# Performance work log

Hardware: AMD Instinct MI355X
Metric: run time of the kernel (lower is better)

Reference implementation:

```python
import jax, jax.numpy as jnp
import numpy as np

B, T, D, V = 32, 384, 768, 32000
PAD = 1
THRESH = 0.95

def setup_inputs() -> dict:
    key = jax.random.key(0)
    ks = jax.random.split(key, 8)
    s = 1.0 / np.sqrt(D)
    sentence = jax.random.randint(ks[0], (B, T), 0, V)
    emb = jax.random.normal(ks[1], (V, D), jnp.float32) * 0.02
    emb = emb.at[PAD].set(0.0)  # padding_idx row is zero
    w_ih = jax.random.uniform(ks[2], (3 * D, D), jnp.float32, -s, s)
    w_hh = jax.random.uniform(ks[3], (3 * D, D), jnp.float32, -s, s)
    b_ih = jax.random.uniform(ks[4], (3 * D,), jnp.float32, -s, s)
    b_hh = jax.random.uniform(ks[5], (3 * D,), jnp.float32, -s, s)
    w_act = jax.random.uniform(ks[6], (D,), jnp.float32, -s, s)
    b_act = jnp.zeros((1,), jnp.float32)
    return dict(sentence=sentence, emb=emb, w_ih=w_ih, w_hh=w_hh,
                b_ih=b_ih, b_hh=b_hh, w_act=w_act, b_act=b_act)


def _gru(x, w_ih, w_hh, b_ih, b_hh):
    # x: [B,T,D] -> states [B,T,D]; PyTorch GRU cell math.
    xp = jnp.einsum('btd,ed->bte', x, w_ih) + b_ih  # [B,T,3D]

    def step(h, xt):
        hp = h @ w_hh.T + b_hh
        xr, xz, xn = jnp.split(xt, 3, axis=-1)
        hr, hz, hn = jnp.split(hp, 3, axis=-1)
        r = jax.nn.sigmoid(xr + hr)
        z = jax.nn.sigmoid(xz + hz)
        n = jnp.tanh(xn + r * hn)
        h_new = (1.0 - z) * n + z * h
        return h_new, h_new

    h0 = jnp.zeros((x.shape[0], w_hh.shape[1]), x.dtype)
    _, hs = jax.lax.scan(step, h0, jnp.swapaxes(xp, 0, 1))
    return jnp.swapaxes(hs, 0, 1)


def _forward(sentence, emb, w_ih, w_hh, b_ih, b_hh, w_act, b_act):
    x = emb[sentence]                                   # [B,T,D]
    states = _gru(x, w_ih, w_hh, b_ih, b_hh)            # [B,T,D]
    probs = jax.nn.sigmoid(states @ w_act + b_act)      # [B,T]

    # ACT-style halting: accumulate probs, emit a segment when sum > threshold.
    def halt_step(hsum, p):
        acc = hsum + p
        halted = acc > THRESH
        return jnp.where(halted, 0.0, acc), halted

    _, halted_t = jax.lax.scan(halt_step, jnp.zeros((B,), probs.dtype), probs.T)
    halted = halted_t.T                                 # [B,T] bool, True at last step of each segment
    h_i = halted.astype(jnp.int32)
    seg_id = jnp.cumsum(h_i, axis=1) - h_i              # exclusive cumsum: segment index per step

    segsum = jax.vmap(lambda v, s: jax.ops.segment_sum(v, s, num_segments=T))
    sum_p = segsum(probs, seg_id)                       # [B,T] per-segment prob sum
    sum_p_at = jnp.take_along_axis(sum_p, seg_id, axis=1)
    # last step of a segment gets weight p_last - stopgrad(sum_seg - 1)
    weights = jnp.where(halted, probs - jax.lax.stop_gradient(sum_p_at - 1.0), probs)
    seg_embs = segsum(states * weights[..., None], seg_id)  # [B,T,D]

    n_segs = h_i.sum(axis=1)                            # [B] completed segments
    valid = jnp.arange(T)[None, :] < n_segs[:, None]    # [B,T]
    embs = jnp.where(valid[..., None], seg_embs, 0.0)   # zero-pad incomplete slots
    embs = embs.reshape(B * T, D)                       # concat padded per-batch lists
    return embs, probs[..., None]


def reference(sentence, emb, w_ih, w_hh, b_ih, b_hh, w_act, b_act):
    return _forward(sentence, emb, w_ih, w_hh, b_ih, b_hh, w_act, b_act)
```

## Files before the change

### kernel.cpp

```cpp
#include <hip/hip_runtime.h>
#include <math.h>

#define BATCH 32
#define SEQT 384
#define DIM 768
#define D3 2304
#define NROWS (BATCH*SEQT)
#define VTHRESH 0.95f

typedef float  f32x4 __attribute__((ext_vector_type(4)));

#define OFF_XP   ((size_t)0)
#define SZ_XP    ((size_t)NROWS * D3 * 4)
#define OFF_ST   (OFF_XP + SZ_XP)
#define SZ_ST    ((size_t)NROWS * DIM * 4)
#define OFF_PR   (OFF_ST + SZ_ST)
#define SZ_PR    ((size_t)NROWS * 4)
#define OFF_WT   (OFF_PR + SZ_PR)
#define OFF_SS   (OFF_WT + SZ_PR)
#define OFF_SE   (OFF_SS + SZ_PR)
#define OFF_NS   (OFF_SE + SZ_PR)
#define OFF_HB   (OFF_NS + 256)
#define NBG 8
#define BPG 4
#define WPB 32
#define CPW 24
#define BGBYTES ((size_t)(DIM * 2 * 16))
#define SZ_HB   ((size_t)2 * NBG * BGBYTES)
#define INIT_FLOATS (SZ_HB/4)

#define DOT4(a,b) ((a).x*(b).x + (a).y*(b).y + (a).z*(b).z + (a).w*(b).w)

__global__ __launch_bounds__(256, 2) void k_xp(
    const int* __restrict__ sent, const float* __restrict__ emb,
    const float* __restrict__ w_ih, const float* __restrict__ b_ih,
    float* __restrict__ xp)
{
    __shared__ float As[16][132];
    __shared__ float Bs[16][132];
    const int tid = threadIdx.x;
    const int mt = blockIdx.x, nt = blockIdx.y;
    const int tx = tid & 15, ty = tid >> 4;
    const int lm = tid >> 2;
    const int lk = (tid & 3) << 2;

    const long arow0 = (long)sent[mt*128 + lm] * DIM;
    const long arow1 = (long)sent[mt*128 + lm + 64] * DIM;
    const float* b0p = w_ih + (size_t)(nt*128 + lm) * DIM;
    const float* b1p = w_ih + (size_t)(nt*128 + lm + 64) * DIM;

    float acc[8][8];
    #pragma unroll
    for (int i = 0; i < 8; ++i)
        #pragma unroll
        for (int j = 0; j < 8; ++j) acc[i][j] = 0.f;

    for (int k0 = 0; k0 < DIM; k0 += 16) {
        float4 a0 = *(const float4*)(emb + arow0 + k0 + lk);
        float4 a1 = *(const float4*)(emb + arow1 + k0 + lk);
        float4 b0 = *(const float4*)(b0p + k0 + lk);
        float4 b1 = *(const float4*)(b1p + k0 + lk);
        __syncthreads();
        As[lk+0][lm] = a0.x; As[lk+1][lm] = a0.y; As[lk+2][lm] = a0.z; As[lk+3][lm] = a0.w;
        As[lk+0][lm+64] = a1.x; As[lk+1][lm+64] = a1.y; As[lk+2][lm+64] = a1.z; As[lk+3][lm+64] = a1.w;
        Bs[lk+0][lm] = b0.x; Bs[lk+1][lm] = b0.y; Bs[lk+2][lm] = b0.z; Bs[lk+3][lm] = b0.w;
        Bs[lk+0][lm+64] = b1.x; Bs[lk+1][lm+64] = b1.y; Bs[lk+2][lm+64] = b1.z; Bs[lk+3][lm+64] = b1.w;
        __syncthreads();
        #pragma unroll
        for (int k = 0; k < 16; ++k) {
            float4 av0 = *(const float4*)&As[k][ty*8];
            float4 av1 = *(const float4*)&As[k][ty*8+4];
            float4 bv0 = *(const float4*)&Bs[k][tx*8];
            float4 bv1 = *(const float4*)&Bs[k][tx*8+4];
            float a[8] = {av0.x,av0.y,av0.z,av0.w,av1.x,av1.y,av1.z,av1.w};
            float b[8] = {bv0.x,bv0.y,bv0.z,bv0.w,bv1.x,bv1.y,bv1.z,bv1.w};
            #pragma unroll
            for (int i = 0; i < 8; ++i)
                #pragma unroll
                for (int j = 0; j < 8; ++j)
                    acc[i][j] += a[i]*b[j];
        }
    }

    const int m0 = mt*128 + ty*8;
    const int n0 = nt*128 + tx*8;
    float4 bi0 = *(const float4*)(b_ih + n0);
    float4 bi1 = *(const float4*)(b_ih + n0 + 4);
    #pragma unroll
    for (int i = 0; i < 8; ++i) {
        float4 v0, v1;
        v0.x = acc[i][0] + bi0.x; v0.y = acc[i][1] + bi0.y;
        v0.z = acc[i][2] + bi0.z; v0.w = acc[i][3] + bi0.w;
        v1.x = acc[i][4] + bi1.x; v1.y = acc[i][5] + bi1.y;
        v1.z = acc[i][6] + bi1.z; v1.w = acc[i][7] + bi1.w;
        *(float4*)(xp + (size_t)(m0+i)*D3 + n0)     = v0;
        *(float4*)(xp + (size_t)(m0+i)*D3 + n0 + 4) = v1;
    }
}

#define HPITCH 772

__global__ __launch_bounds__(768, 1) void k_gru(
    const float* __restrict__ w_hh, const float* __restrict__ b_hh,
    const float* __restrict__ xp, float* __restrict__ states,
    char* __restrict__ hbuf)
{
    __shared__ float h_lds[2][BPG][HPITCH];

    const int tid = threadIdx.x;
    const int jb  = blockIdx.x & 31;
    const int bg  = blockIdx.x >> 5;
    const int w    = tid >> 6;
    const int lane = tid & 63;
    const int half = lane >> 5;
    const int c32  = lane & 31;
    const int col  = jb*CPW + w*2 + half;
    const int bloc = (c32 >> 3) & 3;
    const int batch = bg*BPG + bloc;

    f32x4 w4[3][6];
    #pragma unroll
    for (int g3 = 0; g3 < 3; ++g3) {
        const float* wr = w_hh + (size_t)(g3*DIM + col)*DIM + c32*4;
        #pragma unroll
        for (int m = 0; m < 6; ++m)
            w4[g3][m] = *(const f32x4*)(wr + m*128);
    }
    const float bhr = b_hh[col];
    const float bhz = b_hh[DIM + col];
    const float bhn = b_hh[2*DIM + col];

    int goff[2], ldsoff[2], onemask = 0;
    #pragma unroll
    for (int i = 0; i < 2; ++i) {
        int q = i*768 + tid;
        int cq = q >> 1, sq = q & 1;
        goff[i]   = q << 4;
        ldsoff[i] = (sq ? 3 : 0)*HPITCH + cq;
        if (sq) onemask |= (1<<i);
    }

    char* pb[2];
    pb[0] = hbuf + (size_t)(0*NBG + bg)*BGBYTES;
    pb[1] = hbuf + (size_t)(1*NBG + bg)*BGBYTES;

    const float* xq = xp + (size_t)batch*SEQT*D3 + col;

    f32x4 ch[2];

#define ISSUE_POLLS(pbx)                                                 \
    {                                                                    \
        _Pragma("unroll")                                                \
        for (int k = 0; k < 2; ++k) {                                    \
            const f32x4* ap = (const f32x4*)((pbx) + goff[k]);           \
            asm volatile("global_load_dwordx4 %0, %1, off sc0 sc1"       \
                         : "=v"(ch[k]) : "v"(ap));                       \
        }                                                                \
    }

#define WAIT_FILL(pbx, hb0, tt)                                          \
    {                                                                    \
        asm volatile("s_waitcnt vmcnt(0)" ::: "memory");                 \
        __builtin_amdgcn_sched_barrier(0);                               \
        int need = 3;                                                    \
        _Pragma("unroll")                                                \
        for (int k = 0; k < 2; ++k)                                      \
            if (__float_as_int(ch[k].w) == (tt)) need &= ~(1<<k);        \
        while (need) {                                                   \
            _Pragma("unroll")                                            \
            for (int k = 0; k < 2; ++k)                                  \
                if (need & (1<<k)) {                                     \
                    const f32x4* ap = (const f32x4*)((pbx) + goff[k]);   \
                    asm volatile("global_load_dwordx4 %0, %1, off sc0 sc1"\
                                 : "=v"(ch[k]) : "v"(ap));               \
                }                                                        \
            asm volatile("s_waitcnt vmcnt(0)" ::: "memory");             \
            __builtin_amdgcn_sched_barrier(0);                           \
            _Pragma("unroll")                                            \
            for (int k = 0; k < 2; ++k)                                  \
                if ((need & (1<<k)) && __float_as_int(ch[k].w) == (tt))  \
                    need &= ~(1<<k);                                     \
            if (need) __builtin_amdgcn_s_sleep(1);                       \
        }                                                                \
        _Pragma("unroll")                                                \
        for (int k = 0; k < 2; ++k) {                                    \
            (hb0)[ldsoff[k]] = ch[k].x;                                  \
            if (!((onemask >> k) & 1)) {                                 \
                (hb0)[ldsoff[k] + HPITCH]   = ch[k].y;                   \
                (hb0)[ldsoff[k] + 2*HPITCH] = ch[k].z;                   \
            }                                                            \
        }                                                                \
    }

#define GRU_GATES(xr, xz, xn, ar, az, an)                                \
    {                                                                    \
        float rg = 1.f / (1.f + expf(-((xr) + (ar) + bhr)));             \
        float zg = 1.f / (1.f + expf(-((xz) + (az) + bhz)));             \
        float ng = tanhf((xn) + rg * ((an) + bhn));                      \
        hold = (1.f - zg) * ng + zg * hold;                              \
    }

#define PUBLISH(pbx, tt)                                                 \
    {                                                                    \
        int gp = (lane >> 1) & 1;                                        \
        int sq = lane & 1;                                               \
        float q0 = __shfl(hold, gp*32 + (sq ? 24 : 0));                  \
        float q1 = __shfl(hold, gp*32 + 8);                              \
        float q2 = __shfl(hold, gp*32 + 16);                             \
        if (lane < 4) {                                                  \
            f32x4 val;                                                   \
            val.x = q0; val.y = q1; val.z = q2;                          \
            val.w = __int_as_float((tt) + 1);                            \
            int colp = jb*CPW + w*2 + gp;                                \
            f32x4* ap = (f32x4*)((pbx) + (size_t)(colp*2 + sq)*16);      \
            asm volatile("global_store_dwordx4 %0, %1, off sc0 sc1"      \
                         :: "v"(ap), "v"(val) : "memory");               \
        }                                                                \
        if ((c32 & 7) == 0)                                              \
            states[(size_t)(batch*SEQT + (tt))*DIM + col] = hold;        \
    }

    float hold = 0.f;

    float xr = xq[0], xz = xq[DIM], xn = xq[2*DIM];
    GRU_GATES(xr, xz, xn, 0.f, 0.f, 0.f);
    PUBLISH(pb[0], 0);
    ISSUE_POLLS(pb[0]);
    float xrn = xq[(size_t)D3], xzn = xq[(size_t)D3 + DIM],
          xnn = xq[(size_t)D3 + 2*DIM];

    for (int t = 1; t < SEQT; ++t) {
        float* hb0 = &h_lds[t & 1][0][0];
        WAIT_FILL(pb[(t-1)&1], hb0, t);
        xr = xrn; xz = xzn; xn = xnn;
        if (t + 1 < SEQT) {
            xrn = xq[(size_t)(t+1)*D3];
            xzn = xq[(size_t)(t+1)*D3 + DIM];
            xnn = xq[(size_t)(t+1)*D3 + 2*DIM];
        }
        __syncthreads();

        float v[12];
        #pragma unroll
        for (int i = 0; i < 12; ++i) v[i] = 0.f;
        const float* hk = hb0 + c32*4;
        #pragma unroll
        for (int bb = 0; bb < 4; ++bb) {
            const float* hr = hk + bb*HPITCH;
            #pragma unroll
            for (int m = 0; m < 6; ++m) {
                f32x4 h4 = *(const f32x4*)(hr + m*128);
                v[bb*3+0] += DOT4(h4, w4[0][m]);
                v[bb*3+1] += DOT4(h4, w4[1][m]);
                v[bb*3+2] += DOT4(h4, w4[2][m]);
            }
        }
        #pragma unroll
        for (int i = 0; i < 6; ++i) {
            float send = (c32 & 16) ? v[i] : v[i+6];
            float keep = (c32 & 16) ? v[i+6] : v[i];
            v[i] = keep + __shfl_xor(send, 16);
        }
        #pragma unroll
        for (int i = 0; i < 3; ++i) {
            float send = (c32 & 8) ? v[i] : v[i+3];
            float keep = (c32 & 8) ? v[i+3] : v[i];
            v[i] = keep + __shfl_xor(send, 8);
        }
        #pragma unroll
        for (int i = 0; i < 3; ++i) v[i] += __shfl_xor(v[i], 4);
        #pragma unroll
        for (int i = 0; i < 3; ++i) v[i] += __shfl_xor(v[i], 2);
        #pragma unroll
        for (int i = 0; i < 3; ++i) v[i] += __shfl_xor(v[i], 1);

        GRU_GATES(xr, xz, xn, v[0], v[1], v[2]);
        PUBLISH(pb[t&1], t);
        if (t + 1 < SEQT)
            ISSUE_POLLS(pb[t&1]);
    }
#undef ISSUE_POLLS
#undef WAIT_FILL
#undef GRU_GATES
#undef PUBLISH
}

__global__ __launch_bounds__(256, 4) void k_probs(
    const float* __restrict__ states, const float* __restrict__ w_act,
    const float* __restrict__ b_act, float* __restrict__ probs,
    float* __restrict__ out_probs)
{
    int row  = blockIdx.x*4 + (threadIdx.x >> 6);
    int lane = threadIdx.x & 63;
    const float* sr = states + (size_t)row * DIM;
    float s = 0.f;
    #pragma unroll
    for (int i = 0; i < 3; ++i) {
        float4 v = *(const float4*)(sr + i*256 + lane*4);
        float4 w = *(const float4*)(w_act + i*256 + lane*4);
        s += v.x*w.x + v.y*w.y + v.z*w.z + v.w*w.w;
    }
    #pragma unroll
    for (int off = 32; off > 0; off >>= 1) s += __shfl_xor(s, off);
    if (lane == 0) {
        float pv = 1.f / (1.f + expf(-(s + b_act[0])));
        probs[row]     = pv;
        out_probs[row] = pv;
    }
}

__global__ void k_scan(const float* __restrict__ probs, float* __restrict__ weights,
                       int* __restrict__ seg_start, int* __restrict__ seg_end,
                       int* __restrict__ n_segs)
{
    int b = threadIdx.x;
    if (b >= BATCH) return;
    float acc = 0.f;
    int s = 0, start = 0;
    for (int t0 = 0; t0 < SEQT; t0 += 4) {
        float4 p4 = *(const float4*)(probs + b*SEQT + t0);
        float pv[4] = {p4.x, p4.y, p4.z, p4.w};
        #pragma unroll
        for (int k = 0; k < 4; ++k) {
            int t = t0 + k;
            float pp = pv[k];
            acc += pp;
            float w = pp;
            if (acc > VTHRESH) {
                w = pp - (acc - 1.0f);
                seg_start[b*SEQT + s] = start;
                seg_end[b*SEQT + s]   = t;
                s++; start = t + 1; acc = 0.f;
            }
            weights[b*SEQT + t] = w;
        }
    }
    n_segs[b] = s;
}

__global__ __launch_bounds__(256, 4) void k_embs(
    const float* __restrict__ states, const float* __restrict__ weights,
    const int* __restrict__ seg_start, const int* __restrict__ seg_end,
    const int* __restrict__ n_segs, float* __restrict__ out)
{
    int r = blockIdx.x;
    int b = r / SEQT;
    int s = r - b*SEQT;
    int tid = threadIdx.x;
    float a0 = 0.f, a1 = 0.f, a2 = 0.f;
    if (s < n_segs[b]) {
        int st = seg_start[r], en = seg_end[r];
        for (int t = st; t <= en; ++t) {
            float w = weights[b*SEQT + t];
            const float* sp = states + (size_t)(b*SEQT + t) * DIM;
            a0 += w * sp[tid];
            a1 += w * sp[tid + 256];
            a2 += w * sp[tid + 512];
        }
    }
    float* o = out + (size_t)r * DIM;
    o[tid]       = a0;
    o[tid + 256] = a1;
    o[tid + 512] = a2;
}

__global__ void k_init(float* hb) {
    int i = blockIdx.x * 256 + threadIdx.x;
    if (i < INIT_FLOATS) hb[i] = 0.f;
}

extern "C" void kernel_launch(void* const* d_in, const int* in_sizes, int n_in,
                              void* d_out, int out_size, void* d_ws, size_t ws_size,
                              hipStream_t stream)
{
    const int*   sent  = (const int*)d_in[0];
    const float* emb   = (const float*)d_in[1];
    const float* w_ih  = (const float*)d_in[2];
    const float* w_hh  = (const float*)d_in[3];
    const float* b_ih  = (const float*)d_in[4];
    const float* b_hh  = (const float*)d_in[5];
    const float* w_act = (const float*)d_in[6];
    const float* b_act = (const float*)d_in[7];
    float* out = (float*)d_out;

    char* ws = (char*)d_ws;
    float* xp      = (float*)(ws + OFF_XP);
    float* states  = (float*)(ws + OFF_ST);
    float* probs   = (float*)(ws + OFF_PR);
    float* weights = (float*)(ws + OFF_WT);
    int*   sstart  = (int*)(ws + OFF_SS);
    int*   send    = (int*)(ws + OFF_SE);
    int*   nsegs   = (int*)(ws + OFF_NS);
    char*  hbuf    = (char*)(ws + OFF_HB);

    k_init<<<384, 256, 0, stream>>>((float*)hbuf);
    k_xp<<<dim3(96, 18), 256, 0, stream>>>(sent, emb, w_ih, b_ih, xp);
    k_gru<<<256, 768, 0, stream>>>(w_hh, b_hh, xp, states, hbuf);
    k_probs<<<NROWS/4, 256, 0, stream>>>(states, w_act, b_act, probs,
                                         out + (size_t)NROWS * DIM);
    k_scan<<<1, 64, 0, stream>>>(probs, weights, sstart, send, nsegs);
    k_embs<<<NROWS, 256, 0, stream>>>(states, weights, sstart, send, nsegs, out);
}
```

Baseline: 2.334 ms.

## Split recurrent matvec to overlap second-half hidden-state polling with compute

The per-step wait for the published hidden state is split in two. The block waits for the first half of the chunks, computes the partial matvec over those columns (m=0..2), and only then finishes polling the second half before computing the rest. This is meant to hide cross-block synchronization latency on the serial GRU critical path. The gate math also switches to raw v_exp_f32/v_rcp_f32 approximations instead of expf/tanhf, and weight loads go through inline asm with an explicit wait. The change adds a second __syncthreads per step and slightly lowers precision in the gates.

```diff
diff --git a/kernel.cpp b/kernel.cpp
--- a/kernel.cpp
+++ b/kernel.cpp
@@ -31,6 +31,14 @@
 
 #define DOT4(a,b) ((a).x*(b).x + (a).y*(b).y + (a).z*(b).z + (a).w*(b).w)
 
+__device__ __forceinline__ float fexp2(float x) {
+    float r; asm("v_exp_f32 %0, %1" : "=v"(r) : "v"(x)); return r;
+}
+__device__ __forceinline__ float frcp(float x) {
+    float r; asm("v_rcp_f32 %0, %1" : "=v"(r) : "v"(x)); return r;
+}
+#define LOG2E 1.44269504f
+
 __global__ __launch_bounds__(256, 2) void k_xp(
     const int* __restrict__ sent, const float* __restrict__ emb,
     const float* __restrict__ w_ih, const float* __restrict__ b_ih,
@@ -123,9 +131,15 @@
     for (int g3 = 0; g3 < 3; ++g3) {
         const float* wr = w_hh + (size_t)(g3*DIM + col)*DIM + c32*4;
         #pragma unroll
-        for (int m = 0; m < 6; ++m)
-            w4[g3][m] = *(const f32x4*)(wr + m*128);
-    }
+        for (int m = 0; m < 6; ++m) {
+            const f32x4* ap = (const f32x4*)(wr + m*128);
+            asm volatile("global_load_dwordx4 %0, %1, off"
+                         : "=v"(w4[g3][m]) : "v"(ap));
+        }
+    }
+    asm volatile("s_waitcnt vmcnt(0)" ::: "memory");
+    __builtin_amdgcn_sched_barrier(0);
+
     const float bhr = b_hh[col];
     const float bhz = b_hh[DIM + col];
     const float bhn = b_hh[2*DIM + col];
@@ -158,45 +172,12 @@
         }                                                                \
     }
 
-#define WAIT_FILL(pbx, hb0, tt)                                          \
-    {                                                                    \
-        asm volatile("s_waitcnt vmcnt(0)" ::: "memory");                 \
-        __builtin_amdgcn_sched_barrier(0);                               \
-        int need = 3;                                                    \
-        _Pragma("unroll")                                                \
-        for (int k = 0; k < 2; ++k)                                      \
-            if (__float_as_int(ch[k].w) == (tt)) need &= ~(1<<k);        \
-        while (need) {                                                   \
-            _Pragma("unroll")                                            \
-            for (int k = 0; k < 2; ++k)                                  \
-                if (need & (1<<k)) {                                     \
-                    const f32x4* ap = (const f32x4*)((pbx) + goff[k]);   \
-                    asm volatile("global_load_dwordx4 %0, %1, off sc0 sc1"\
-                                 : "=v"(ch[k]) : "v"(ap));               \
-                }                                                        \
-            asm volatile("s_waitcnt vmcnt(0)" ::: "memory");             \
-            __builtin_amdgcn_sched_barrier(0);                           \
-            _Pragma("unroll")                                            \
-            for (int k = 0; k < 2; ++k)                                  \
-                if ((need & (1<<k)) && __float_as_int(ch[k].w) == (tt))  \
-                    need &= ~(1<<k);                                     \
-            if (need) __builtin_amdgcn_s_sleep(1);                       \
-        }                                                                \
-        _Pragma("unroll")                                                \
-        for (int k = 0; k < 2; ++k) {                                    \
-            (hb0)[ldsoff[k]] = ch[k].x;                                  \
-            if (!((onemask >> k) & 1)) {                                 \
-                (hb0)[ldsoff[k] + HPITCH]   = ch[k].y;                   \
-                (hb0)[ldsoff[k] + 2*HPITCH] = ch[k].z;                   \
-            }                                                            \
-        }                                                                \
-    }
-
 #define GRU_GATES(xr, xz, xn, ar, az, an)                                \
     {                                                                    \
-        float rg = 1.f / (1.f + expf(-((xr) + (ar) + bhr)));             \
-        float zg = 1.f / (1.f + expf(-((xz) + (az) + bhz)));             \
-        float ng = tanhf((xn) + rg * ((an) + bhn));                      \
+        float rg = frcp(1.f + fexp2(-LOG2E*((xr) + (ar) + bhr)));        \
+        float zg = frcp(1.f + fexp2(-LOG2E*((xz) + (az) + bhz)));        \
+        float sn = (xn) + rg * ((an) + bhn);                             \
+        float ng = 1.f - 2.f*frcp(1.f + fexp2(2.f*LOG2E*sn));            \
         hold = (1.f - zg) * ng + zg * hold;                              \
     }
 
@@ -231,24 +212,92 @@
 
     for (int t = 1; t < SEQT; ++t) {
         float* hb0 = &h_lds[t & 1][0][0];
-        WAIT_FILL(pb[(t-1)&1], hb0, t);
+        const char* pbx = pb[(t-1)&1];
+
+        asm volatile("s_waitcnt vmcnt(0)" ::: "memory");
+        __builtin_amdgcn_sched_barrier(0);
+        bool up_ok = (__float_as_int(ch[1].w) == t);
+        while (__float_as_int(ch[0].w) != t) {
+            __builtin_amdgcn_s_sleep(1);
+            {
+                const f32x4* a0 = (const f32x4*)(pbx + goff[0]);
+                asm volatile("global_load_dwordx4 %0, %1, off sc0 sc1"
+                             : "=v"(ch[0]) : "v"(a0));
+            }
+            if (!up_ok) {
+                const f32x4* a1 = (const f32x4*)(pbx + goff[1]);
+                asm volatile("global_load_dwordx4 %0, %1, off sc0 sc1"
+                             : "=v"(ch[1]) : "v"(a1));
+            }
+            asm volatile("s_waitcnt vmcnt(0)" ::: "memory");
+            __builtin_amdgcn_sched_barrier(0);
+            if (!up_ok) up_ok = (__float_as_int(ch[1].w) == t);
+        }
+        hb0[ldsoff[0]] = ch[0].x;
+        if (!(onemask & 1)) {
+            hb0[ldsoff[0] + HPITCH]   = ch[0].y;
+            hb0[ldsoff[0] + 2*HPITCH] = ch[0].z;
+        }
+        if (up_ok) {
+            hb0[ldsoff[1]] = ch[1].x;
+            if (!(onemask & 2)) {
+                hb0[ldsoff[1] + HPITCH]   = ch[1].y;
+                hb0[ldsoff[1] + 2*HPITCH] = ch[1].z;
+            }
+        } else {
+            const f32x4* a1 = (const f32x4*)(pbx + goff[1]);
+            asm volatile("global_load_dwordx4 %0, %1, off sc0 sc1"
+                         : "=v"(ch[1]) : "v"(a1));
+        }
         xr = xrn; xz = xzn; xn = xnn;
+        __syncthreads();
+
+        float v[12];
+        #pragma unroll
+        for (int i = 0; i < 12; ++i) v[i] = 0.f;
+        const float* hk = hb0 + c32*4;
+        #pragma unroll
+        for (int bb = 0; bb < 4; ++bb) {
+            const float* hr = hk + bb*HPITCH;
+            #pragma unroll
+            for (int m = 0; m < 3; ++m) {
+                f32x4 h4 = *(const f32x4*)(hr + m*128);
+                v[bb*3+0] += DOT4(h4, w4[0][m]);
+                v[bb*3+1] += DOT4(h4, w4[1][m]);
+                v[bb*3+2] += DOT4(h4, w4[2][m]);
+            }
+        }
+
+        if (!up_ok) {
+            asm volatile("s_waitcnt vmcnt(0)" ::: "memory");
+            __builtin_amdgcn_sched_barrier(0);
+            while (__float_as_int(ch[1].w) != t) {
+                __builtin_amdgcn_s_sleep(1);
+                const f32x4* a1 = (const f32x4*)(pbx + goff[1]);
+                asm volatile("global_load_dwordx4 %0, %1, off sc0 sc1"
+                             : "=v"(ch[1]) : "v"(a1));
+                asm volatile("s_waitcnt vmcnt(0)" ::: "memory");
+                __builtin_amdgcn_sched_barrier(0);
+            }
+            hb0[ldsoff[1]] = ch[1].x;
+            if (!(onemask & 2)) {
+                hb0[ldsoff[1] + HPITCH]   = ch[1].y;
+                hb0[ldsoff[1] + 2*HPITCH] = ch[1].z;
+            }
+        }
+        __syncthreads();
+
         if (t + 1 < SEQT) {
             xrn = xq[(size_t)(t+1)*D3];
             xzn = xq[(size_t)(t+1)*D3 + DIM];
             xnn = xq[(size_t)(t+1)*D3 + 2*DIM];
         }
-        __syncthreads();
-
-        float v[12];
-        #pragma unroll
-        for (int i = 0; i < 12; ++i) v[i] = 0.f;
-        const float* hk = hb0 + c32*4;
+
         #pragma unroll
         for (int bb = 0; bb < 4; ++bb) {
             const float* hr = hk + bb*HPITCH;
             #pragma unroll
-            for (int m = 0; m < 6; ++m) {
+            for (int m = 3; m < 6; ++m) {
                 f32x4 h4 = *(const f32x4*)(hr + m*128);
                 v[bb*3+0] += DOT4(h4, w4[0][m]);
                 v[bb*3+1] += DOT4(h4, w4[1][m]);
@@ -280,7 +329,6 @@
             ISSUE_POLLS(pb[t&1]);
     }
 #undef ISSUE_POLLS
-#undef WAIT_FILL
 #undef GRU_GATES
 #undef PUBLISH
 }
```

New measurement: 2.197 ms. 5.8% less time.
